# Kernel optimization log

Hardware: AMD Instinct MI355X
Metric: run time of the kernel (lower is better)

Reference implementation:

```python
import jax, jax.numpy as jnp
import numpy as np

N_NODES = 40000
N_EDGES = 640000
D = 128


def setup_inputs() -> dict:
    key = jax.random.key(0)
    ks = jax.random.split(key, 7)
    x = jax.random.normal(ks[0], (N_NODES, D), dtype=jnp.float32)
    edge_index = jax.random.randint(ks[1], (2, N_EDGES), 0, N_NODES, dtype=jnp.int64)
    # uniform in [0.5, 1.5) to avoid division blow-up near zero
    edge_attr = jax.random.uniform(ks[2], (N_EDGES,), dtype=jnp.float32) + 0.5
    s = 1.0 / np.sqrt(D)
    W1 = jax.random.uniform(ks[3], (D, D), dtype=jnp.float32, minval=-s, maxval=s)
    b1 = jax.random.uniform(ks[4], (D,), dtype=jnp.float32, minval=-s, maxval=s)
    W2 = jax.random.uniform(ks[5], (D, D), dtype=jnp.float32, minval=-s, maxval=s)
    b2 = jax.random.uniform(ks[6], (D,), dtype=jnp.float32, minval=-s, maxval=s)
    return {"x": x, "edge_index": edge_index, "edge_attr": edge_attr,
            "W1": W1, "b1": b1, "W2": W2, "b2": b2}


def _layer(x, src, dst, edge_attr, W, b, num_nodes):
    # message: gather source features, divide by per-edge scalar
    msg = x[src] / edge_attr[:, None]                      # [E, D]
    # aggregate: scatter-add into destination nodes
    agg = jax.ops.segment_sum(msg, dst, num_segments=num_nodes)  # [N, D]
    # linear (torch: y = x @ W.T + b) then leaky_relu(0.01)
    y = agg @ W.T + b
    return jnp.where(y >= 0, y, 0.01 * y)


def reference(x, edge_index, edge_attr, W1, b1, W2, b2):
    src, dst = edge_index[0], edge_index[1]
    n = x.shape[0]
    x = jnp.maximum(_layer(x, src, dst, edge_attr, W1, b1, n), 0.0)
    x = jnp.maximum(_layer(x, src, dst, edge_attr, W2, b2, n), 0.0)
    return x
```

## Files before the change

### kernel.cpp

```cpp
#include <hip/hip_runtime.h>

#define D 128
#define CAP 64
typedef unsigned short u16;
typedef unsigned int   u32;

typedef __attribute__((ext_vector_type(8))) short short8;
typedef __attribute__((ext_vector_type(4))) float f32x4;

__device__ __forceinline__ u32 f2bf(float f) {
    u32 u = __float_as_uint(f);
    u += 0x7fffu + ((u >> 16) & 1u);
    return u >> 16;
}
__device__ __forceinline__ float2 bf2x2(u32 u) {
    float2 r;
    r.x = __uint_as_float(u << 16);
    r.y = __uint_as_float(u & 0xffff0000u);
    return r;
}

__global__ __launch_bounds__(256) void prep_kernel(
    const float4* __restrict__ x, uint2* __restrict__ xb,
    const float4* __restrict__ W1, const float4* __restrict__ W2,
    uint2* __restrict__ wb1, uint2* __restrict__ wb2,
    const int* __restrict__ src, const int* __restrict__ dst,
    const float* __restrict__ attr, int* __restrict__ counts,
    u32* __restrict__ combo, int E, int n4, int cvtb, int Nper, int N)
{
    const int bid = blockIdx.x;
    const int t   = threadIdx.x;

    if (bid < cvtb) {
        int i = bid * 256 + t;
        if (i < n4) {
            float4 v = x[i];
            uint2 o;
            o.x = f2bf(v.x) | (f2bf(v.y) << 16);
            o.y = f2bf(v.z) | (f2bf(v.w) << 16);
            xb[i] = o;
        }
    } else if (bid < cvtb + 32) {
        int i = (bid - cvtb) * 256 + t;
        const float4* in = (i < 4096) ? W1 : W2;
        uint2* out = (i < 4096) ? wb1 : wb2;
        int k = i & 4095;
        float4 v = in[k];
        uint2 o;
        o.x = f2bf(v.x) | (f2bf(v.y) << 16);
        o.y = f2bf(v.z) | (f2bf(v.w) << 16);
        out[k] = o;
    } else {
        const int sb    = bid - cvtb - 32;
        const int xcd   = sb & 7;
        const int chunk = sb >> 3;
        const int lo    = xcd * Nper;
        const int hi    = min(lo + Nper, N);
        long long e0 = (long long)chunk * 1024 + t * 4;

        if (e0 + 3 < E) {
            int4   s4 = *(const int4*)(src + e0);
            int4   d4 = *(const int4*)(dst + e0);
            float4 a4 = *(const float4*)(attr + e0);
            #pragma unroll
            for (int q = 0; q < 4; ++q) {
                int d = (q == 0) ? d4.x : (q == 1) ? d4.y : (q == 2) ? d4.z : d4.w;
                if (d >= lo && d < hi) {
                    int s = (q == 0) ? s4.x : (q == 1) ? s4.y : (q == 2) ? s4.z : s4.w;
                    float a = (q == 0) ? a4.x : (q == 1) ? a4.y : (q == 2) ? a4.z : a4.w;
                    int r = atomicAdd(&counts[d], 1);
                    if (r < CAP)
                        combo[((long long)d << 6) + r] =
                            (u32)s | (f2bf(1.0f / a) << 16);
                }
            }
        } else {
            for (int q = 0; q < 4; ++q) {
                long long e = e0 + q;
                if (e < E) {
                    int d = dst[e];
                    if (d >= lo && d < hi) {
                        int r = atomicAdd(&counts[d], 1);
                        if (r < CAP)
                            combo[((long long)d << 6) + r] =
                                (u32)src[e] | (f2bf(1.0f / attr[e]) << 16);
                    }
                }
            }
        }
    }
}

__global__ __launch_bounds__(256) void gather_kernel(
    const u16* __restrict__ x, const u32* __restrict__ combo,
    const int* __restrict__ counts, u16* __restrict__ agg, int Nper, int N)
{
    const int xcd   = blockIdx.x & 7;
    const int slice = blockIdx.x >> 3;
    const int node  = xcd * Nper + slice * 4 + (threadIdx.x >> 6);
    if (node >= N || (slice * 4 + (threadIdx.x >> 6)) >= Nper) return;
    const int lane = threadIdx.x & 63;

    const int cnt = min(counts[node], CAP);
    const u32 ce = combo[((long long)node << 6) + lane];

    float2 acc[8];
    #pragma unroll
    for (int q = 0; q < 8; ++q) acc[q] = {0.f, 0.f};

    int j = 0;
    for (; j + 7 < cnt; j += 8) {
        u32 ed[8], rw[8];
        #pragma unroll
        for (int q = 0; q < 8; ++q) ed[q] = __shfl(ce, j + q);
        #pragma unroll
        for (int q = 0; q < 8; ++q)
            rw[q] = *(const u32*)(x + (long long)(ed[q] & 0xffffu) * D + lane * 2);
        #pragma unroll
        for (int q = 0; q < 8; ++q) {
            float f = __uint_as_float(ed[q] & 0xffff0000u);
            float2 v = bf2x2(rw[q]);
            acc[q].x += v.x * f; acc[q].y += v.y * f;
        }
    }
    for (; j + 3 < cnt; j += 4) {
        u32 ed[4], rw[4];
        #pragma unroll
        for (int q = 0; q < 4; ++q) ed[q] = __shfl(ce, j + q);
        #pragma unroll
        for (int q = 0; q < 4; ++q)
            rw[q] = *(const u32*)(x + (long long)(ed[q] & 0xffffu) * D + lane * 2);
        #pragma unroll
        for (int q = 0; q < 4; ++q) {
            float f = __uint_as_float(ed[q] & 0xffff0000u);
            float2 v = bf2x2(rw[q]);
            acc[q].x += v.x * f; acc[q].y += v.y * f;
        }
    }
    for (; j < cnt; ++j) {
        u32 e = __shfl(ce, j);
        u32 r = *(const u32*)(x + (long long)(e & 0xffffu) * D + lane * 2);
        float f = __uint_as_float(e & 0xffff0000u);
        float2 v = bf2x2(r);
        acc[0].x += v.x * f; acc[0].y += v.y * f;
    }

    float s0 = ((acc[0].x + acc[1].x) + (acc[2].x + acc[3].x))
             + ((acc[4].x + acc[5].x) + (acc[6].x + acc[7].x));
    float s1 = ((acc[0].y + acc[1].y) + (acc[2].y + acc[3].y))
             + ((acc[4].y + acc[5].y) + (acc[6].y + acc[7].y));
    u32 o = f2bf(s0) | (f2bf(s1) << 16);
    *(u32*)(agg + (long long)node * D + lane * 2) = o;
}

template <bool OUT_BF16>
__global__ __launch_bounds__(256) void mfma_gemm_kernel(
    const u16* __restrict__ A, const u16* __restrict__ Wb,
    const float* __restrict__ b, void* __restrict__ Yv, int N)
{
    const int wv   = threadIdx.x >> 6;
    const int lane = threadIdx.x & 63;
    const int m0   = (blockIdx.x * 4 + wv) * 16;
    const int mrow = lane & 15;
    const int kq   = lane >> 4;

    const u16* arow = A + (long long)(m0 + mrow) * D + kq * 8;
    short8 afr[4];
    #pragma unroll
    for (int ks = 0; ks < 4; ++ks)
        afr[ks] = *(const short8*)(arow + ks * 32);

    #pragma unroll 1
    for (int j = 0; j < 8; ++j) {
        float bias = b[j * 16 + mrow];
        f32x4 acc = {bias, bias, bias, bias};
        const u16* wrow = Wb + (long long)(j * 16 + mrow) * D + kq * 8;
        #pragma unroll
        for (int ks = 0; ks < 4; ++ks) {
            short8 bfr = *(const short8*)(wrow + ks * 32);
            acc = __builtin_amdgcn_mfma_f32_16x16x32_bf16(afr[ks], bfr, acc, 0, 0, 0);
        }
        #pragma unroll
        for (int r = 0; r < 4; ++r) {
            float v = acc[r] > 0.f ? acc[r] : 0.f;
            int row = m0 + kq * 4 + r;
            int col = j * 16 + mrow;
            if (OUT_BF16)
                *((u16*)Yv + (long long)row * D + col) = (u16)f2bf(v);
            else
                *((float*)Yv + (long long)row * D + col) = v;
        }
    }
}

extern "C" void kernel_launch(void* const* d_in, const int* in_sizes, int n_in,
                              void* d_out, int out_size, void* d_ws, size_t ws_size,
                              hipStream_t stream)
{
    const float* x    = (const float*)d_in[0];
    const int*   eidx = (const int*)d_in[1];
    const float* attr = (const float*)d_in[2];
    const float* W1   = (const float*)d_in[3];
    const float* b1   = (const float*)d_in[4];
    const float* W2   = (const float*)d_in[5];
    const float* b2   = (const float*)d_in[6];

    const int N = in_sizes[0] / D;
    const int E = in_sizes[2];
    const int* src = eidx;
    const int* dst = eidx + E;
    const int Nper = (N + 7) / 8;

    char* p = (char*)d_ws;
    u16*  xb    = (u16*)p;   p += ((size_t)N * D * 2 + 15) & ~15ULL;
    u16*  aggB  = (u16*)p;   p += ((size_t)N * D * 2 + 15) & ~15ULL;
    u32*  combo = (u32*)p;   p += (size_t)N * CAP * 4;
    u16*  wb1   = (u16*)p;   p += (size_t)D * D * 2;
    u16*  wb2   = (u16*)p;   p += (size_t)D * D * 2;
    int*  counts= (int*)p;

    const int n4    = N * D / 4;
    const int cvtb  = (n4 + 255) / 256;
    const int hfb   = 8 * ((E + 1023) / 1024);
    const int prepb = cvtb + 32 + hfb;
    const int gatherb = 8 * ((Nper + 3) / 4);
    const int gemmb   = (N + 63) / 64;

    hipMemsetAsync(counts, 0, (size_t)N * 4, stream);
    prep_kernel<<<prepb, 256, 0, stream>>>(
        (const float4*)x, (uint2*)xb, (const float4*)W1, (const float4*)W2,
        (uint2*)wb1, (uint2*)wb2, src, dst, attr, counts,
        combo, E, n4, cvtb, Nper, N);

    gather_kernel<<<gatherb, 256, 0, stream>>>(xb, combo, counts, aggB, Nper, N);
    mfma_gemm_kernel<true><<<gemmb, 256, 0, stream>>>(aggB, wb1, b1, aggB, N);

    gather_kernel<<<gatherb, 256, 0, stream>>>(aggB, combo, counts, xb, Nper, N);
    mfma_gemm_kernel<false><<<gemmb, 256, 0, stream>>>(xb, wb2, b2, d_out, N);
}
```

Measured before the change: 194.7 us.

## Fuse all stages into one cooperative persistent kernel with grid syncs

```diff
diff --git a/kernel.cpp b/kernel.cpp
--- a/kernel.cpp
+++ b/kernel.cpp
@@ -1,7 +1,12 @@
 #include <hip/hip_runtime.h>
+#include <hip/hip_cooperative_groups.h>
+
+namespace cg = cooperative_groups;
 
 #define D 128
 #define CAP 64
+#define NTHR 256
+
 typedef unsigned short u16;
 typedef unsigned int   u32;
 
@@ -20,70 +25,74 @@
     return r;
 }
 
-__global__ __launch_bounds__(256) void prep_kernel(
-    const float4* __restrict__ x, uint2* __restrict__ xb,
-    const float4* __restrict__ W1, const float4* __restrict__ W2,
-    uint2* __restrict__ wb1, uint2* __restrict__ wb2,
-    const int* __restrict__ src, const int* __restrict__ dst,
-    const float* __restrict__ attr, int* __restrict__ counts,
-    u32* __restrict__ combo, int E, int n4, int cvtb, int Nper, int N)
-{
-    const int bid = blockIdx.x;
-    const int t   = threadIdx.x;
-
-    if (bid < cvtb) {
-        int i = bid * 256 + t;
-        if (i < n4) {
-            float4 v = x[i];
-            uint2 o;
-            o.x = f2bf(v.x) | (f2bf(v.y) << 16);
-            o.y = f2bf(v.z) | (f2bf(v.w) << 16);
-            xb[i] = o;
-        }
-    } else if (bid < cvtb + 32) {
-        int i = (bid - cvtb) * 256 + t;
-        const float4* in = (i < 4096) ? W1 : W2;
-        uint2* out = (i < 4096) ? wb1 : wb2;
-        int k = i & 4095;
+struct Params {
+    const float4* x;    uint2* xb;
+    const float4* W1;   const float4* W2;
+    uint2* wb1;         uint2* wb2;
+    const int* src;     const int* dst;   const float* attr;
+    int* counts;        u32* combo;
+    const float* b1;    const float* b2;
+    u16* aggB;          float* out;
+    int E, n4, N, Nper;
+};
+
+__device__ __forceinline__ void phase0_body(const Params& p, int gtid, int gsz)
+{
+    for (int i = gtid; i < p.N; i += gsz) p.counts[i] = 0;
+    for (int i = gtid; i < p.n4; i += gsz) {
+        float4 v = p.x[i];
+        uint2 o;
+        o.x = f2bf(v.x) | (f2bf(v.y) << 16);
+        o.y = f2bf(v.z) | (f2bf(v.w) << 16);
+        p.xb[i] = o;
+    }
+    if (gtid < 8192) {
+        const float4* in = (gtid < 4096) ? p.W1 : p.W2;
+        uint2* outw = (gtid < 4096) ? p.wb1 : p.wb2;
+        int k = gtid & 4095;
         float4 v = in[k];
         uint2 o;
         o.x = f2bf(v.x) | (f2bf(v.y) << 16);
         o.y = f2bf(v.z) | (f2bf(v.w) << 16);
-        out[k] = o;
-    } else {
-        const int sb    = bid - cvtb - 32;
-        const int xcd   = sb & 7;
-        const int chunk = sb >> 3;
-        const int lo    = xcd * Nper;
-        const int hi    = min(lo + Nper, N);
+        outw[k] = o;
+    }
+}
+
+__device__ __forceinline__ void histfill_phase(const Params& p, int bid, int t)
+{
+    const int xcd = bid & 7;
+    const int lo  = xcd * p.Nper;
+    const int hi  = min(lo + p.Nper, p.N);
+    const int nchunks = (p.E + 1023) / 1024;
+    const int stride  = gridDim.x >> 3;
+    for (int chunk = bid >> 3; chunk < nchunks; chunk += stride) {
         long long e0 = (long long)chunk * 1024 + t * 4;
-
-        if (e0 + 3 < E) {
-            int4   s4 = *(const int4*)(src + e0);
-            int4   d4 = *(const int4*)(dst + e0);
-            float4 a4 = *(const float4*)(attr + e0);
+        if (e0 + 3 < p.E) {
+            int4   s4 = *(const int4*)(p.src + e0);
+            int4   d4 = *(const int4*)(p.dst + e0);
+            float4 a4 = *(const float4*)(p.attr + e0);
             #pragma unroll
             for (int q = 0; q < 4; ++q) {
                 int d = (q == 0) ? d4.x : (q == 1) ? d4.y : (q == 2) ? d4.z : d4.w;
                 if (d >= lo && d < hi) {
-                    int s = (q == 0) ? s4.x : (q == 1) ? s4.y : (q == 2) ? s4.z : s4.w;
+                    int   s = (q == 0) ? s4.x : (q == 1) ? s4.y : (q == 2) ? s4.z : s4.w;
                     float a = (q == 0) ? a4.x : (q == 1) ? a4.y : (q == 2) ? a4.z : a4.w;
-                    int r = atomicAdd(&counts[d], 1);
+                    int r = atomicAdd(&p.counts[d], 1);
                     if (r < CAP)
-                        combo[((long long)d << 6) + r] =
+                        p.combo[((long long)d << 6) + r] =
                             (u32)s | (f2bf(1.0f / a) << 16);
                 }
             }
         } else {
             for (int q = 0; q < 4; ++q) {
                 long long e = e0 + q;
-                if (e < E) {
-                    int d = dst[e];
+                if (e < p.E) {
+                    int d = p.dst[e];
                     if (d >= lo && d < hi) {
-                        int r = atomicAdd(&counts[d], 1);
+                        int r = atomicAdd(&p.counts[d], 1);
                         if (r < CAP)
-                            combo[((long long)d << 6) + r] =
-                                (u32)src[e] | (f2bf(1.0f / attr[e]) << 16);
+                            p.combo[((long long)d << 6) + r] =
+                                (u32)p.src[e] | (f2bf(1.0f / p.attr[e]) << 16);
                     }
                 }
             }
@@ -91,106 +100,155 @@
     }
 }
 
-__global__ __launch_bounds__(256) void gather_kernel(
-    const u16* __restrict__ x, const u32* __restrict__ combo,
-    const int* __restrict__ counts, u16* __restrict__ agg, int Nper, int N)
-{
-    const int xcd   = blockIdx.x & 7;
-    const int slice = blockIdx.x >> 3;
-    const int node  = xcd * Nper + slice * 4 + (threadIdx.x >> 6);
-    if (node >= N || (slice * 4 + (threadIdx.x >> 6)) >= Nper) return;
-    const int lane = threadIdx.x & 63;
-
-    const int cnt = min(counts[node], CAP);
-    const u32 ce = combo[((long long)node << 6) + lane];
-
-    float2 acc[8];
-    #pragma unroll
-    for (int q = 0; q < 8; ++q) acc[q] = {0.f, 0.f};
-
-    int j = 0;
-    for (; j + 7 < cnt; j += 8) {
-        u32 ed[8], rw[8];
+__device__ __forceinline__ void gather_phase(
+    const u16* __restrict__ X, const u32* __restrict__ combo,
+    const int* __restrict__ counts, u16* __restrict__ agg,
+    int N, int Nper, int bid, int t)
+{
+    const int xcd  = bid & 7;
+    const int lane = t & 63;
+    const int wv   = t >> 6;
+    const int stride = (gridDim.x >> 3) * 4;
+
+    for (int nidx = (bid >> 3) * 4 + wv; nidx < Nper; nidx += stride) {
+        const int node = xcd * Nper + nidx;
+        if (node >= N) continue;
+
+        const int cnt = min(counts[node], CAP);
+        const u32 ce = combo[((long long)node << 6) + lane];
+
+        float2 acc[8];
         #pragma unroll
-        for (int q = 0; q < 8; ++q) ed[q] = __shfl(ce, j + q);
-        #pragma unroll
-        for (int q = 0; q < 8; ++q)
-            rw[q] = *(const u32*)(x + (long long)(ed[q] & 0xffffu) * D + lane * 2);
-        #pragma unroll
-        for (int q = 0; q < 8; ++q) {
-            float f = __uint_as_float(ed[q] & 0xffff0000u);
-            float2 v = bf2x2(rw[q]);
-            acc[q].x += v.x * f; acc[q].y += v.y * f;
-        }
-    }
-    for (; j + 3 < cnt; j += 4) {
-        u32 ed[4], rw[4];
-        #pragma unroll
-        for (int q = 0; q < 4; ++q) ed[q] = __shfl(ce, j + q);
-        #pragma unroll
-        for (int q = 0; q < 4; ++q)
-            rw[q] = *(const u32*)(x + (long long)(ed[q] & 0xffffu) * D + lane * 2);
-        #pragma unroll
-        for (int q = 0; q < 4; ++q) {
-            float f = __uint_as_float(ed[q] & 0xffff0000u);
-            float2 v = bf2x2(rw[q]);
-            acc[q].x += v.x * f; acc[q].y += v.y * f;
-        }
-    }
-    for (; j < cnt; ++j) {
-        u32 e = __shfl(ce, j);
-        u32 r = *(const u32*)(x + (long long)(e & 0xffffu) * D + lane * 2);
-        float f = __uint_as_float(e & 0xffff0000u);
-        float2 v = bf2x2(r);
-        acc[0].x += v.x * f; acc[0].y += v.y * f;
-    }
-
-    float s0 = ((acc[0].x + acc[1].x) + (acc[2].x + acc[3].x))
-             + ((acc[4].x + acc[5].x) + (acc[6].x + acc[7].x));
-    float s1 = ((acc[0].y + acc[1].y) + (acc[2].y + acc[3].y))
-             + ((acc[4].y + acc[5].y) + (acc[6].y + acc[7].y));
-    u32 o = f2bf(s0) | (f2bf(s1) << 16);
-    *(u32*)(agg + (long long)node * D + lane * 2) = o;
+        for (int q = 0; q < 8; ++q) acc[q] = {0.f, 0.f};
+
+        int j = 0;
+        for (; j + 7 < cnt; j += 8) {
+            u32 ed[8], rw[8];
+            #pragma unroll
+            for (int q = 0; q < 8; ++q) ed[q] = __shfl(ce, j + q);
+            #pragma unroll
+            for (int q = 0; q < 8; ++q)
+                rw[q] = *(const u32*)(X + (long long)(ed[q] & 0xffffu) * D + lane * 2);
+            #pragma unroll
+            for (int q = 0; q < 8; ++q) {
+                float f = __uint_as_float(ed[q] & 0xffff0000u);
+                float2 v = bf2x2(rw[q]);
+                acc[q].x += v.x * f; acc[q].y += v.y * f;
+            }
+        }
+        for (; j + 3 < cnt; j += 4) {
+            u32 ed[4], rw[4];
+            #pragma unroll
+            for (int q = 0; q < 4; ++q) ed[q] = __shfl(ce, j + q);
+            #pragma unroll
+            for (int q = 0; q < 4; ++q)
+                rw[q] = *(const u32*)(X + (long long)(ed[q] & 0xffffu) * D + lane * 2);
+            #pragma unroll
+            for (int q = 0; q < 4; ++q) {
+                float f = __uint_as_float(ed[q] & 0xffff0000u);
+                float2 v = bf2x2(rw[q]);
+                acc[q].x += v.x * f; acc[q].y += v.y * f;
+            }
+        }
+        for (; j < cnt; ++j) {
+            u32 e = __shfl(ce, j);
+            u32 r = *(const u32*)(X + (long long)(e & 0xffffu) * D + lane * 2);
+            float f = __uint_as_float(e & 0xffff0000u);
+            float2 v = bf2x2(r);
+            acc[0].x += v.x * f; acc[0].y += v.y * f;
+        }
+
+        float s0 = ((acc[0].x + acc[1].x) + (acc[2].x + acc[3].x))
+                 + ((acc[4].x + acc[5].x) + (acc[6].x + acc[7].x));
+        float s1 = ((acc[0].y + acc[1].y) + (acc[2].y + acc[3].y))
+                 + ((acc[4].y + acc[5].y) + (acc[6].y + acc[7].y));
+        u32 o = f2bf(s0) | (f2bf(s1) << 16);
+        *(u32*)(agg + (long long)node * D + lane * 2) = o;
+    }
 }
 
 template <bool OUT_BF16>
-__global__ __launch_bounds__(256) void mfma_gemm_kernel(
+__device__ __forceinline__ void gemm_phase(
     const u16* __restrict__ A, const u16* __restrict__ Wb,
-    const float* __restrict__ b, void* __restrict__ Yv, int N)
-{
-    const int wv   = threadIdx.x >> 6;
-    const int lane = threadIdx.x & 63;
-    const int m0   = (blockIdx.x * 4 + wv) * 16;
+    const float* __restrict__ bias, void* __restrict__ Yv,
+    int N, int bid, int t)
+{
+    const int lane = t & 63;
     const int mrow = lane & 15;
     const int kq   = lane >> 4;
-
-    const u16* arow = A + (long long)(m0 + mrow) * D + kq * 8;
-    short8 afr[4];
-    #pragma unroll
-    for (int ks = 0; ks < 4; ++ks)
-        afr[ks] = *(const short8*)(arow + ks * 32);
-
-    #pragma unroll 1
-    for (int j = 0; j < 8; ++j) {
-        float bias = b[j * 16 + mrow];
-        f32x4 acc = {bias, bias, bias, bias};
-        const u16* wrow = Wb + (long long)(j * 16 + mrow) * D + kq * 8;
+    const int tiles = (N + 15) >> 4;
+    const int stride = gridDim.x * 4;
+
+    for (int tile = bid * 4 + (t >> 6); tile < tiles; tile += stride) {
+        const int m0 = tile * 16;
+
+        const u16* arow = A + (long long)(m0 + mrow) * D + kq * 8;
+        short8 afr[4];
         #pragma unroll
-        for (int ks = 0; ks < 4; ++ks) {
-            short8 bfr = *(const short8*)(wrow + ks * 32);
-            acc = __builtin_amdgcn_mfma_f32_16x16x32_bf16(afr[ks], bfr, acc, 0, 0, 0);
-        }
-        #pragma unroll
-        for (int r = 0; r < 4; ++r) {
-            float v = acc[r] > 0.f ? acc[r] : 0.f;
-            int row = m0 + kq * 4 + r;
-            int col = j * 16 + mrow;
-            if (OUT_BF16)
-                *((u16*)Yv + (long long)row * D + col) = (u16)f2bf(v);
-            else
-                *((float*)Yv + (long long)row * D + col) = v;
-        }
-    }
+        for (int ks = 0; ks < 4; ++ks)
+            afr[ks] = *(const short8*)(arow + ks * 32);
+
+        #pragma unroll 1
+        for (int j = 0; j < 8; ++j) {
+            float bv = bias[j * 16 + mrow];
+            f32x4 acc = {bv, bv, bv, bv};
+            const u16* wrow = Wb + (long long)(j * 16 + mrow) * D + kq * 8;
+            #pragma unroll
+            for (int ks = 0; ks < 4; ++ks) {
+                short8 bfr = *(const short8*)(wrow + ks * 32);
+                acc = __builtin_amdgcn_mfma_f32_16x16x32_bf16(afr[ks], bfr, acc, 0, 0, 0);
+            }
+            #pragma unroll
+            for (int r = 0; r < 4; ++r) {
+                float v = acc[r] > 0.f ? acc[r] : 0.f;
+                int row = m0 + kq * 4 + r;
+                int col = j * 16 + mrow;
+                if (row < N) {
+                    if (OUT_BF16)
+                        *((u16*)Yv + (long long)row * D + col) = (u16)f2bf(v);
+                    else
+                        *((float*)Yv + (long long)row * D + col) = v;
+                }
+            }
+        }
+    }
+}
+
+__global__ __launch_bounds__(NTHR, 4) void mono_kernel(Params p)
+{
+    cg::grid_group grid = cg::this_grid();
+    const int bid  = blockIdx.x;
+    const int t    = threadIdx.x;
+    const int gtid = bid * NTHR + t;
+    const int gsz  = gridDim.x * NTHR;
+
+    phase0_body(p, gtid, gsz);
+    grid.sync();
+    histfill_phase(p, bid, t);
+    grid.sync();
+    gather_phase((const u16*)p.xb, p.combo, p.counts, p.aggB, p.N, p.Nper, bid, t);
+    grid.sync();
+    gemm_phase<true>(p.aggB, (const u16*)p.wb1, p.b1, p.aggB, p.N, bid, t);
+    grid.sync();
+    gather_phase(p.aggB, p.combo, p.counts, (u16*)p.xb, p.N, p.Nper, bid, t);
+    grid.sync();
+    gemm_phase<false>((const u16*)p.xb, (const u16*)p.wb2, p.b2, p.out, p.N, bid, t);
+}
+
+__global__ __launch_bounds__(NTHR) void k_prep0(Params p) {
+    phase0_body(p, blockIdx.x * NTHR + threadIdx.x, gridDim.x * NTHR);
+}
+__global__ __launch_bounds__(NTHR) void k_hist(Params p) {
+    histfill_phase(p, blockIdx.x, threadIdx.x);
+}
+__global__ __launch_bounds__(NTHR) void k_gather(
+    const u16* X, const u32* combo, const int* counts, u16* agg, int N, int Nper) {
+    gather_phase(X, combo, counts, agg, N, Nper, blockIdx.x, threadIdx.x);
+}
+template <bool OUT_BF16>
+__global__ __launch_bounds__(NTHR) void k_gemm(
+    const u16* A, const u16* Wb, const float* bias, void* Yv, int N) {
+    gemm_phase<OUT_BF16>(A, Wb, bias, Yv, N, blockIdx.x, threadIdx.x);
 }
 
 extern "C" void kernel_launch(void* const* d_in, const int* in_sizes, int n_in,
@@ -207,9 +265,6 @@
 
     const int N = in_sizes[0] / D;
     const int E = in_sizes[2];
-    const int* src = eidx;
-    const int* dst = eidx + E;
-    const int Nper = (N + 7) / 8;
 
     char* p = (char*)d_ws;
     u16*  xb    = (u16*)p;   p += ((size_t)N * D * 2 + 15) & ~15ULL;
@@ -219,22 +274,45 @@
     u16*  wb2   = (u16*)p;   p += (size_t)D * D * 2;
     int*  counts= (int*)p;
 
-    const int n4    = N * D / 4;
-    const int cvtb  = (n4 + 255) / 256;
-    const int hfb   = 8 * ((E + 1023) / 1024);
-    const int prepb = cvtb + 32 + hfb;
-    const int gatherb = 8 * ((Nper + 3) / 4);
+    Params prm;
+    prm.x   = (const float4*)x;   prm.xb  = (uint2*)xb;
+    prm.W1  = (const float4*)W1;  prm.W2  = (const float4*)W2;
+    prm.wb1 = (uint2*)wb1;        prm.wb2 = (uint2*)wb2;
+    prm.src = eidx;               prm.dst = eidx + E;
+    prm.attr = attr;
+    prm.counts = counts;          prm.combo = combo;
+    prm.b1 = b1;                  prm.b2 = b2;
+    prm.aggB = aggB;              prm.out = (float*)d_out;
+    prm.E = E;                    prm.n4 = N * D / 4;
+    prm.N = N;                    prm.Nper = (N + 7) / 8;
+
+    hipError_t st = hipErrorUnknown;
+    int maxBpc = 0;
+    if (hipOccupancyMaxActiveBlocksPerMultiprocessor(
+            &maxBpc, (const void*)mono_kernel, NTHR, 0) == hipSuccess && maxBpc > 0) {
+        int dev = 0;
+        hipGetDevice(&dev);
+        hipDeviceProp_t props;
+        if (hipGetDeviceProperties(&props, dev) == hipSuccess) {
+            int bpc  = maxBpc < 4 ? maxBpc : 4;
+            int grid = bpc * props.multiProcessorCount;
+            if (grid >= 64 && (grid & 7) == 0) {
+                void* args[] = { (void*)&prm };
+                st = hipLaunchCooperativeKernel((const void*)mono_kernel,
+                                                dim3(grid), dim3(NTHR),
+                                                args, 0, stream);
+            }
+        }
+    }
+    if (st == hipSuccess) return;
+
+    const int hfb     = 8 * ((E + 1023) / 1024);
+    const int gatherb = 8 * ((prm.Nper + 3) / 4);
     const int gemmb   = (N + 63) / 64;
-
-    hipMemsetAsync(counts, 0, (size_t)N * 4, stream);
-    prep_kernel<<<prepb, 256, 0, stream>>>(
-        (const float4*)x, (uint2*)xb, (const float4*)W1, (const float4*)W2,
-        (uint2*)wb1, (uint2*)wb2, src, dst, attr, counts,
-        combo, E, n4, cvtb, Nper, N);
-
-    gather_kernel<<<gatherb, 256, 0, stream>>>(xb, combo, counts, aggB, Nper, N);
-    mfma_gemm_kernel<true><<<gemmb, 256, 0, stream>>>(aggB, wb1, b1, aggB, N);
-
-    gather_kernel<<<gatherb, 256, 0, stream>>>(aggB, combo, counts, xb, Nper, N);
-    mfma_gemm_kernel<false><<<gemmb, 256, 0, stream>>>(xb, wb2, b2, d_out, N);
-}
+    k_prep0<<<5000, NTHR, 0, stream>>>(prm);
+    k_hist<<<hfb, NTHR, 0, stream>>>(prm);
+    k_gather<<<gatherb, NTHR, 0, stream>>>((const u16*)xb, combo, counts, aggB, N, prm.Nper);
+    k_gemm<true><<<gemmb, NTHR, 0, stream>>>(aggB, (const u16*)wb1, b1, aggB, N);
+    k_gather<<<gatherb, NTHR, 0, stream>>>(aggB, combo, counts, xb, N, prm.Nper);
+    k_gemm<false><<<gemmb, NTHR, 0, stream>>>((const u16*)xb, (const u16*)wb2, b2, d_out, N);
+}
```

Result: slower. 684.5 us (+251.6%).

## Apply linear transform before aggregation and fuse bias/relu into gather epilogue

Applied to the files above, without the earlier changes.

```diff
diff --git a/kernel.cpp b/kernel.cpp
--- a/kernel.cpp
+++ b/kernel.cpp
@@ -19,41 +19,30 @@
     r.y = __uint_as_float(u & 0xffff0000u);
     return r;
 }
+__device__ __forceinline__ short8 pack_bf8(const float* p) {
+    float4 a = *(const float4*)p;
+    float4 b = *(const float4*)(p + 4);
+    uint4 u;
+    u.x = f2bf(a.x) | (f2bf(a.y) << 16);
+    u.y = f2bf(a.z) | (f2bf(a.w) << 16);
+    u.z = f2bf(b.x) | (f2bf(b.y) << 16);
+    u.w = f2bf(b.z) | (f2bf(b.w) << 16);
+    return *(short8*)&u;
+}
 
 __global__ __launch_bounds__(256) void prep_kernel(
-    const float4* __restrict__ x, uint2* __restrict__ xb,
-    const float4* __restrict__ W1, const float4* __restrict__ W2,
-    uint2* __restrict__ wb1, uint2* __restrict__ wb2,
+    const float* __restrict__ x, const float* __restrict__ W1,
+    u16* __restrict__ z0,
     const int* __restrict__ src, const int* __restrict__ dst,
     const float* __restrict__ attr, int* __restrict__ counts,
-    u32* __restrict__ combo, int E, int n4, int cvtb, int Nper, int N)
+    u32* __restrict__ combo, int E, int hfb, int Nper, int N)
 {
     const int bid = blockIdx.x;
     const int t   = threadIdx.x;
 
-    if (bid < cvtb) {
-        int i = bid * 256 + t;
-        if (i < n4) {
-            float4 v = x[i];
-            uint2 o;
-            o.x = f2bf(v.x) | (f2bf(v.y) << 16);
-            o.y = f2bf(v.z) | (f2bf(v.w) << 16);
-            xb[i] = o;
-        }
-    } else if (bid < cvtb + 32) {
-        int i = (bid - cvtb) * 256 + t;
-        const float4* in = (i < 4096) ? W1 : W2;
-        uint2* out = (i < 4096) ? wb1 : wb2;
-        int k = i & 4095;
-        float4 v = in[k];
-        uint2 o;
-        o.x = f2bf(v.x) | (f2bf(v.y) << 16);
-        o.y = f2bf(v.z) | (f2bf(v.w) << 16);
-        out[k] = o;
-    } else {
-        const int sb    = bid - cvtb - 32;
-        const int xcd   = sb & 7;
-        const int chunk = sb >> 3;
+    if (bid < hfb) {
+        const int xcd   = bid & 7;
+        const int chunk = bid >> 3;
         const int lo    = xcd * Nper;
         const int hi    = min(lo + Nper, N);
         long long e0 = (long long)chunk * 1024 + t * 4;
@@ -66,7 +55,7 @@
             for (int q = 0; q < 4; ++q) {
                 int d = (q == 0) ? d4.x : (q == 1) ? d4.y : (q == 2) ? d4.z : d4.w;
                 if (d >= lo && d < hi) {
-                    int s = (q == 0) ? s4.x : (q == 1) ? s4.y : (q == 2) ? s4.z : s4.w;
+                    int   s = (q == 0) ? s4.x : (q == 1) ? s4.y : (q == 2) ? s4.z : s4.w;
                     float a = (q == 0) ? a4.x : (q == 1) ? a4.y : (q == 2) ? a4.z : a4.w;
                     int r = atomicAdd(&counts[d], 1);
                     if (r < CAP)
@@ -88,17 +77,50 @@
                 }
             }
         }
-    }
-}
-
+    } else {
+        const int wv   = t >> 6;
+        const int lane = t & 63;
+        const int m0   = ((bid - hfb) * 4 + wv) * 16;
+        const int mrow = lane & 15;
+        const int kq   = lane >> 4;
+
+        const float* arow = x + (long long)(m0 + mrow) * D + kq * 8;
+        short8 afr[4];
+        #pragma unroll
+        for (int ks = 0; ks < 4; ++ks)
+            afr[ks] = pack_bf8(arow + ks * 32);
+
+        #pragma unroll 1
+        for (int j = 0; j < 8; ++j) {
+            f32x4 acc = {0.f, 0.f, 0.f, 0.f};
+            const float* wrow = W1 + (long long)(j * 16 + mrow) * D + kq * 8;
+            #pragma unroll
+            for (int ks = 0; ks < 4; ++ks) {
+                short8 bfr = pack_bf8(wrow + ks * 32);
+                acc = __builtin_amdgcn_mfma_f32_16x16x32_bf16(afr[ks], bfr, acc, 0, 0, 0);
+            }
+            #pragma unroll
+            for (int r = 0; r < 4; ++r) {
+                int row = m0 + kq * 4 + r;
+                int col = j * 16 + mrow;
+                z0[(long long)row * D + col] = (u16)f2bf(acc[r]);
+            }
+        }
+    }
+}
+
+template <bool OUT_BF16>
 __global__ __launch_bounds__(256) void gather_kernel(
-    const u16* __restrict__ x, const u32* __restrict__ combo,
-    const int* __restrict__ counts, u16* __restrict__ agg, int Nper, int N)
+    const u16* __restrict__ z, const u32* __restrict__ combo,
+    const int* __restrict__ counts, const float* __restrict__ bias,
+    void* __restrict__ Yv, int Nper, int N)
 {
     const int xcd   = blockIdx.x & 7;
     const int slice = blockIdx.x >> 3;
-    const int node  = xcd * Nper + slice * 4 + (threadIdx.x >> 6);
-    if (node >= N || (slice * 4 + (threadIdx.x >> 6)) >= Nper) return;
+    const int nidx  = slice * 4 + (threadIdx.x >> 6);
+    if (nidx >= Nper) return;
+    const int node = xcd * Nper + nidx;
+    if (node >= N) return;
     const int lane = threadIdx.x & 63;
 
     const int cnt = min(counts[node], CAP);
@@ -115,7 +137,7 @@
         for (int q = 0; q < 8; ++q) ed[q] = __shfl(ce, j + q);
         #pragma unroll
         for (int q = 0; q < 8; ++q)
-            rw[q] = *(const u32*)(x + (long long)(ed[q] & 0xffffu) * D + lane * 2);
+            rw[q] = *(const u32*)(z + (long long)(ed[q] & 0xffffu) * D + lane * 2);
         #pragma unroll
         for (int q = 0; q < 8; ++q) {
             float f = __uint_as_float(ed[q] & 0xffff0000u);
@@ -129,7 +151,7 @@
         for (int q = 0; q < 4; ++q) ed[q] = __shfl(ce, j + q);
         #pragma unroll
         for (int q = 0; q < 4; ++q)
-            rw[q] = *(const u32*)(x + (long long)(ed[q] & 0xffffu) * D + lane * 2);
+            rw[q] = *(const u32*)(z + (long long)(ed[q] & 0xffffu) * D + lane * 2);
         #pragma unroll
         for (int q = 0; q < 4; ++q) {
             float f = __uint_as_float(ed[q] & 0xffff0000u);
@@ -139,7 +161,7 @@
     }
     for (; j < cnt; ++j) {
         u32 e = __shfl(ce, j);
-        u32 r = *(const u32*)(x + (long long)(e & 0xffffu) * D + lane * 2);
+        u32 r = *(const u32*)(z + (long long)(e & 0xffffu) * D + lane * 2);
         float f = __uint_as_float(e & 0xffff0000u);
         float2 v = bf2x2(r);
         acc[0].x += v.x * f; acc[0].y += v.y * f;
@@ -149,14 +171,22 @@
              + ((acc[4].x + acc[5].x) + (acc[6].x + acc[7].x));
     float s1 = ((acc[0].y + acc[1].y) + (acc[2].y + acc[3].y))
              + ((acc[4].y + acc[5].y) + (acc[6].y + acc[7].y));
-    u32 o = f2bf(s0) | (f2bf(s1) << 16);
-    *(u32*)(agg + (long long)node * D + lane * 2) = o;
-}
-
-template <bool OUT_BF16>
-__global__ __launch_bounds__(256) void mfma_gemm_kernel(
-    const u16* __restrict__ A, const u16* __restrict__ Wb,
-    const float* __restrict__ b, void* __restrict__ Yv, int N)
+    const float2 bb = *(const float2*)(bias + lane * 2);
+    s0 += bb.x; s1 += bb.y;
+    s0 = s0 > 0.f ? s0 : 0.f;
+    s1 = s1 > 0.f ? s1 : 0.f;
+    if (OUT_BF16) {
+        u32 o = f2bf(s0) | (f2bf(s1) << 16);
+        *(u32*)((u16*)Yv + (long long)node * D + lane * 2) = o;
+    } else {
+        float2 o = {s0, s1};
+        *(float2*)((float*)Yv + (long long)node * D + lane * 2) = o;
+    }
+}
+
+__global__ __launch_bounds__(256) void gemm_kernel(
+    const u16* __restrict__ A, const float* __restrict__ W,
+    u16* __restrict__ Z, int N)
 {
     const int wv   = threadIdx.x >> 6;
     const int lane = threadIdx.x & 63;
@@ -172,23 +202,18 @@
 
     #pragma unroll 1
     for (int j = 0; j < 8; ++j) {
-        float bias = b[j * 16 + mrow];
-        f32x4 acc = {bias, bias, bias, bias};
-        const u16* wrow = Wb + (long long)(j * 16 + mrow) * D + kq * 8;
+        f32x4 acc = {0.f, 0.f, 0.f, 0.f};
+        const float* wrow = W + (long long)(j * 16 + mrow) * D + kq * 8;
         #pragma unroll
         for (int ks = 0; ks < 4; ++ks) {
-            short8 bfr = *(const short8*)(wrow + ks * 32);
+            short8 bfr = pack_bf8(wrow + ks * 32);
             acc = __builtin_amdgcn_mfma_f32_16x16x32_bf16(afr[ks], bfr, acc, 0, 0, 0);
         }
         #pragma unroll
         for (int r = 0; r < 4; ++r) {
-            float v = acc[r] > 0.f ? acc[r] : 0.f;
             int row = m0 + kq * 4 + r;
             int col = j * 16 + mrow;
-            if (OUT_BF16)
-                *((u16*)Yv + (long long)row * D + col) = (u16)f2bf(v);
-            else
-                *((float*)Yv + (long long)row * D + col) = v;
+            Z[(long long)row * D + col] = (u16)f2bf(acc[r]);
         }
     }
 }
@@ -212,29 +237,25 @@
     const int Nper = (N + 7) / 8;
 
     char* p = (char*)d_ws;
-    u16*  xb    = (u16*)p;   p += ((size_t)N * D * 2 + 15) & ~15ULL;
-    u16*  aggB  = (u16*)p;   p += ((size_t)N * D * 2 + 15) & ~15ULL;
+    u16*  z0    = (u16*)p;   p += ((size_t)N * D * 2 + 15) & ~15ULL;
+    u16*  y1    = (u16*)p;   p += ((size_t)N * D * 2 + 15) & ~15ULL;
     u32*  combo = (u32*)p;   p += (size_t)N * CAP * 4;
-    u16*  wb1   = (u16*)p;   p += (size_t)D * D * 2;
-    u16*  wb2   = (u16*)p;   p += (size_t)D * D * 2;
     int*  counts= (int*)p;
 
-    const int n4    = N * D / 4;
-    const int cvtb  = (n4 + 255) / 256;
     const int hfb   = 8 * ((E + 1023) / 1024);
-    const int prepb = cvtb + 32 + hfb;
+    const int gemmb = (N + 63) / 64;
+    const int prepb = hfb + gemmb;
     const int gatherb = 8 * ((Nper + 3) / 4);
-    const int gemmb   = (N + 63) / 64;
 
     hipMemsetAsync(counts, 0, (size_t)N * 4, stream);
     prep_kernel<<<prepb, 256, 0, stream>>>(
-        (const float4*)x, (uint2*)xb, (const float4*)W1, (const float4*)W2,
-        (uint2*)wb1, (uint2*)wb2, src, dst, attr, counts,
-        combo, E, n4, cvtb, Nper, N);
-
-    gather_kernel<<<gatherb, 256, 0, stream>>>(xb, combo, counts, aggB, Nper, N);
-    mfma_gemm_kernel<true><<<gemmb, 256, 0, stream>>>(aggB, wb1, b1, aggB, N);
-
-    gather_kernel<<<gatherb, 256, 0, stream>>>(aggB, combo, counts, xb, Nper, N);
-    mfma_gemm_kernel<false><<<gemmb, 256, 0, stream>>>(xb, wb2, b2, d_out, N);
-}
+        x, W1, z0, src, dst, attr, counts, combo, E, hfb, Nper, N);
+
+    gather_kernel<true><<<gatherb, 256, 0, stream>>>(
+        z0, combo, counts, b1, y1, Nper, N);
+
+    gemm_kernel<<<gemmb, 256, 0, stream>>>(y1, W2, z0 , N);
+
+    gather_kernel<false><<<gatherb, 256, 0, stream>>>(
+        z0, combo, counts, b2, d_out, Nper, N);
+}
```

Measured after the change: 235.6 us. 1.21x slower.
